# Kernel tuning notes

Measured on AMD Instinct MI355X. Metric: run time of the kernel, lower is better.

The kernel has to match this reference:

```python
import jax, jax.numpy as jnp
import numpy as np

N_NODES = 100000
N_EDGES = 3200000
NFEAT, NHID, NCLASS = 256, 128, 16


def setup_inputs() -> dict:
    key = jax.random.key(0)
    ks = jax.random.split(key, 7)
    features = jax.random.normal(ks[0], (N_NODES, NFEAT), dtype=jnp.float32)
    edge_index = jax.random.randint(ks[1], (2, N_EDGES), 0, N_NODES, dtype=jnp.int32)
    edge_weight = jax.random.uniform(ks[2], (N_EDGES,), dtype=jnp.float32)
    s1 = 1.0 / np.sqrt(NFEAT)
    s2 = 1.0 / np.sqrt(NHID)
    W1 = jax.random.uniform(ks[3], (NFEAT, NHID), dtype=jnp.float32, minval=-s1, maxval=s1)
    b1 = jax.random.uniform(ks[4], (NHID,), dtype=jnp.float32, minval=-s1, maxval=s1)
    W2 = jax.random.uniform(ks[5], (NHID, NCLASS), dtype=jnp.float32, minval=-s2, maxval=s2)
    b2 = jax.random.uniform(ks[6], (NCLASS,), dtype=jnp.float32, minval=-s2, maxval=s2)
    return {"features": features, "edge_index": edge_index, "edge_weight": edge_weight,
            "W1": W1, "b1": b1, "W2": W2, "b2": b2}


def _sgconv(x, edge_index, edge_weight, W, b, num_nodes):
    # gcn_norm with self-loops (PyG default for SGConv, K=1)
    row, col = edge_index[0], edge_index[1]
    loop = jnp.arange(num_nodes, dtype=row.dtype)
    row = jnp.concatenate([row, loop])
    col = jnp.concatenate([col, loop])
    ew = jnp.concatenate([edge_weight, jnp.ones((num_nodes,), edge_weight.dtype)])
    deg = jax.ops.segment_sum(ew, col, num_segments=num_nodes)
    dinv = jnp.where(deg > 0, jax.lax.rsqrt(deg), 0.0)
    norm = dinv[row] * ew * dinv[col]                       # [E+N]
    msg = x[row] * norm[:, None]                            # gather + scale
    out = jax.ops.segment_sum(msg, col, num_segments=num_nodes)  # scatter-add to targets
    return out @ W + b


def reference(features, edge_index, edge_weight, W1, b1, W2, b2):
    n = features.shape[0]
    h = jax.nn.relu(_sgconv(features, edge_index, edge_weight, W1, b1, n))
    # dropout is identity in eval mode (training=False)
    h = _sgconv(h, edge_index, edge_weight, W2, b2, n)
    return jax.nn.log_softmax(h, axis=1)
```

## Files before the change

### kernel.cpp

```cpp
#include <hip/hip_runtime.h>
#include <hip/hip_bf16.h>

typedef unsigned short u16;
typedef unsigned char u8;
typedef short bf16x8 __attribute__((ext_vector_type(8)));
typedef float f32x4 __attribute__((ext_vector_type(4)));
typedef float f32x2 __attribute__((ext_vector_type(2)));

__device__ __forceinline__ float blo(unsigned u) { return __uint_as_float(u << 16); }
__device__ __forceinline__ float bhi(unsigned u) { return __uint_as_float(u & 0xFFFF0000u); }
__device__ __forceinline__ u16 f2bf(float f) {
    unsigned x = __float_as_uint(f);
    x += 0x7fffu + ((x >> 16) & 1u);
    return (u16)(x >> 16);
}
__device__ __forceinline__ u8 f2fp8(float f) {
    return (u8)(__builtin_amdgcn_cvt_pk_fp8_f32(f, f, 0, false) & 0xFF);
}

#define CAP 80
#define NB_SHIFT 7
#define BNODES 128
#define CAPB 4608
#define MAXNB 800
#define PK 136
#define EPB 4096


__global__ __launch_bounds__(256) void k_prepw(const float* __restrict__ W1, u16* __restrict__ W1t) {
    int t = blockIdx.x * 256 + threadIdx.x;
    int k = t >> 5;
    int n4 = (t & 31) * 4;
    float4 v = *(const float4*)(W1 + k * 128 + n4);
    W1t[(n4 + 0) * 256 + k] = f2bf(v.x);
    W1t[(n4 + 1) * 256 + k] = f2bf(v.y);
    W1t[(n4 + 2) * 256 + k] = f2bf(v.z);
    W1t[(n4 + 3) * 256 + k] = f2bf(v.w);
}


__global__ __launch_bounds__(512) void k_bin(const int* __restrict__ row, const int* __restrict__ col,
                                             const float* __restrict__ ew, int* __restrict__ gcount,
                                             int2* __restrict__ binned, int E, int NB) {
    __shared__ int cl[MAXNB];
    int t = threadIdx.x;
    int base = blockIdx.x * EPB;
    for (int i = t; i < NB; i += 512) cl[i] = 0;
    __syncthreads();

    int e0 = base + t * 8;
    bool full = (e0 + 8 <= E);
    int cs[8];
    if (full) {
        int4 c0 = *(const int4*)(col + e0);
        int4 c1 = *(const int4*)(col + e0 + 4);
        cs[0] = c0.x; cs[1] = c0.y; cs[2] = c0.z; cs[3] = c0.w;
        cs[4] = c1.x; cs[5] = c1.y; cs[6] = c1.z; cs[7] = c1.w;
#pragma unroll
        for (int j = 0; j < 8; ++j) atomicAdd(&cl[cs[j] >> NB_SHIFT], 1);
    } else {
#pragma unroll
        for (int j = 0; j < 8; ++j) {
            int e = e0 + j;
            cs[j] = (e < E) ? col[e] : 0;
            if (e < E) atomicAdd(&cl[cs[j] >> NB_SHIFT], 1);
        }
    }
    __syncthreads();

    for (int b = t; b < NB; b += 512) {
        int c = cl[b];
        cl[b] = (c > 0) ? atomicAdd(gcount + b, c) : 0;
    }
    __syncthreads();

    if (full) {
        int4 r0 = *(const int4*)(row + e0);
        int4 r1 = *(const int4*)(row + e0 + 4);
        float4 w0 = *(const float4*)(ew + e0);
        float4 w1 = *(const float4*)(ew + e0 + 4);
        int rs[8] = {r0.x, r0.y, r0.z, r0.w, r1.x, r1.y, r1.z, r1.w};
        float wv[8] = {w0.x, w0.y, w0.z, w0.w, w1.x, w1.y, w1.z, w1.w};
#pragma unroll
        for (int j = 0; j < 8; ++j) {
            int c = cs[j];
            int b = c >> NB_SHIFT;
            int slot = atomicAdd(&cl[b], 1);
            if (slot < CAPB)
                binned[(size_t)b * CAPB + slot] =
                    make_int2(rs[j] | ((c & (BNODES - 1)) << 20), __float_as_int(wv[j]));
        }
    } else {
#pragma unroll
        for (int j = 0; j < 8; ++j) {
            int e = e0 + j;
            if (e < E) {
                int c = cs[j];
                int b = c >> NB_SHIFT;
                int slot = atomicAdd(&cl[b], 1);
                if (slot < CAPB)
                    binned[(size_t)b * CAPB + slot] =
                        make_int2(row[e] | ((c & (BNODES - 1)) << 20), __float_as_int(ew[e]));
            }
        }
    }
}


__global__ __launch_bounds__(512) void k_fill(const int* __restrict__ gcount, const int2* __restrict__ binned,
                                              int* __restrict__ cnt, float* __restrict__ dinv,
                                              int2* __restrict__ ell, int N, int NB) {
    __shared__ int   c128[BNODES];
    __shared__ float d128[BNODES];
    int t = threadIdx.x;
    int b = blockIdx.x;
    if (t < BNODES) { c128[t] = 0; d128[t] = 0.f; }
    __syncthreads();
    int M = min(gcount[b], CAPB);
    int nb0 = b << NB_SHIFT;
    const int2* src = binned + (size_t)b * CAPB;
    for (int j = t; j < M; j += 512) {
        int2 rec = src[j];
        int r  = rec.x & 0xFFFFF;
        int lc = rec.x >> 20;
        int slot = atomicAdd(&c128[lc], 1);
        if (slot < CAP) ell[(size_t)(nb0 + lc) * CAP + slot] = make_int2(r, rec.y);
        atomicAdd(&d128[lc], __int_as_float(rec.y));
    }
    __syncthreads();
    if (t < BNODES) {
        int n = nb0 + t;
        if (n < N) {
            cnt[n]  = c128[t];
            dinv[n] = rsqrtf(1.0f + d128[t]);
        }
    }
}


__global__ __launch_bounds__(256) void k_gemm1(const float* __restrict__ feat, const u16* __restrict__ W1t,
                                               const float* __restrict__ dinv, u8* __restrict__ h0f, int N) {
    __shared__ u16 As[64 * PK];
    __shared__ u16 Bs[128 * PK];
    int t = threadIdx.x;
    int nb0 = blockIdx.x * 64;
    int wv = t >> 6, lane = t & 63;
    int m16 = lane & 15, quad = lane >> 4;

    f32x4 zero4 = {0.f, 0.f, 0.f, 0.f};
    f32x4 acc[8];
#pragma unroll
    for (int i = 0; i < 8; ++i) acc[i] = zero4;

    for (int half = 0; half < 2; ++half) {
        int k0 = half * 128;
#pragma unroll
        for (int i = 0; i < 8; ++i) {
            int idx = t + 256 * i;
            int r = idx >> 5;
            int c4 = idx & 31;
            int gn = nb0 + r;
            float4 v = (gn < N) ? *(const float4*)(feat + (size_t)gn * 256 + k0 + c4 * 4)
                                : make_float4(0.f, 0.f, 0.f, 0.f);
            ushort4 o;
            o.x = f2bf(v.x); o.y = f2bf(v.y); o.z = f2bf(v.z); o.w = f2bf(v.w);
            *(ushort4*)(As + r * PK + c4 * 4) = o;
        }
#pragma unroll
        for (int i = 0; i < 8; ++i) {
            int idx = t + 256 * i;
            int r = idx >> 4;
            int c = (idx & 15) * 8;
            *(uint4*)(Bs + r * PK + c) = *(const uint4*)(W1t + r * 256 + k0 + c);
        }
        __syncthreads();
        const u16* arow = As + (wv * 16 + m16) * PK + quad * 8;
        const u16* brow = Bs + m16 * PK + quad * 8;
#pragma unroll
        for (int kc = 0; kc < 4; ++kc) {
            bf16x8 a = *(const bf16x8*)(arow + kc * 32);
#pragma unroll
            for (int tn = 0; tn < 8; ++tn) {
                bf16x8 b = *(const bf16x8*)(brow + tn * 16 * PK + kc * 32);
                acc[tn] = __builtin_amdgcn_mfma_f32_16x16x32_bf16(a, b, acc[tn], 0, 0, 0);
            }
        }
        __syncthreads();
    }
    int node0 = nb0 + wv * 16 + quad * 4;
    float dv[4];
#pragma unroll
    for (int r = 0; r < 4; ++r) dv[r] = (node0 + r < N) ? dinv[node0 + r] : 0.f;
#pragma unroll
    for (int tn = 0; tn < 8; ++tn) {
        int hid = tn * 16 + m16;
#pragma unroll
        for (int r = 0; r < 4; ++r) {
            int gn = node0 + r;
            if (gn < N) h0f[(size_t)gn * 128 + hid] = f2fp8(acc[tn][r] * dv[r]);
        }
    }
}


__global__ __launch_bounds__(256) void k_agg1(const u8* __restrict__ h0f, const float* __restrict__ dinv,
                                              const int* __restrict__ cnt, const int2* __restrict__ ell,
                                              const float* __restrict__ b1, const float* __restrict__ W2,
                                              u16* __restrict__ h2b, int N) {
    __shared__ float s_row[16][132];
    __shared__ float s_w2[2048];
    int t = threadIdx.x;
    int wv = t >> 6, lane = t & 63;
    int g = lane >> 4;
    int fl = lane & 15;
    int f = fl * 8;
    int ln = wv * 4 + g;
    int n = blockIdx.x * 16 + ln;
    bool active = n < N;

    {
        float4 wa = *(const float4*)(W2 + t * 8);
        float4 wb = *(const float4*)(W2 + t * 8 + 4);
        *(float4*)&s_w2[t * 8]     = wa;
        *(float4*)&s_w2[t * 8 + 4] = wb;
    }

    f32x2 acc2[4];
#pragma unroll
    for (int j = 0; j < 4; ++j) acc2[j] = (f32x2){0.f, 0.f};

#define ACC8P(V, W)                                                                  \
    {                                                                                \
        f32x2 wv2 = {(W), (W)};                                                      \
        acc2[0] += __builtin_amdgcn_cvt_pk_f32_fp8((V).x, false) * wv2;              \
        acc2[1] += __builtin_amdgcn_cvt_pk_f32_fp8((V).x, true)  * wv2;              \
        acc2[2] += __builtin_amdgcn_cvt_pk_f32_fp8((V).y, false) * wv2;              \
        acc2[3] += __builtin_amdgcn_cvt_pk_f32_fp8((V).y, true)  * wv2;              \
    }

    if (active) {
        float dn = dinv[n];
        {
            uint2 sv = *(const uint2*)(h0f + (size_t)n * 128 + f);
            ACC8P(sv, dn);
        }
        int m = min(cnt[n], CAP);
        const int2* ep = ell + (size_t)n * CAP;
        int k = 0;
        for (; k + 3 < m; k += 4) {
            int4 e01 = *(const int4*)(ep + k);
            int4 e23 = *(const int4*)(ep + k + 2);
            uint2 v0 = *(const uint2*)(h0f + (size_t)e01.x * 128 + f);
            uint2 v1 = *(const uint2*)(h0f + (size_t)e01.z * 128 + f);
            uint2 v2 = *(const uint2*)(h0f + (size_t)e23.x * 128 + f);
            uint2 v3 = *(const uint2*)(h0f + (size_t)e23.z * 128 + f);
            float w0 = __int_as_float(e01.y) * dn;
            float w1 = __int_as_float(e01.w) * dn;
            float w2x = __int_as_float(e23.y) * dn;
            float w3 = __int_as_float(e23.w) * dn;
            ACC8P(v0, w0);
            ACC8P(v1, w1);
            ACC8P(v2, w2x);
            ACC8P(v3, w3);
        }
        for (; k < m; ++k) {
            int2 e = ep[k];
            float w = __int_as_float(e.y) * dn;
            uint2 v = *(const uint2*)(h0f + (size_t)e.x * 128 + f);
            ACC8P(v, w);
        }
        float4 bA = *(const float4*)(b1 + f);
        float4 bB = *(const float4*)(b1 + f + 4);
        float4 oA, oB;
        oA.x = fmaxf(acc2[0][0] + bA.x, 0.f); oA.y = fmaxf(acc2[0][1] + bA.y, 0.f);
        oA.z = fmaxf(acc2[1][0] + bA.z, 0.f); oA.w = fmaxf(acc2[1][1] + bA.w, 0.f);
        oB.x = fmaxf(acc2[2][0] + bB.x, 0.f); oB.y = fmaxf(acc2[2][1] + bB.y, 0.f);
        oB.z = fmaxf(acc2[3][0] + bB.z, 0.f); oB.w = fmaxf(acc2[3][1] + bB.w, 0.f);
        *(float4*)&s_row[ln][f]     = oA;
        *(float4*)&s_row[ln][f + 4] = oB;
    }
#undef ACC8P
    __syncthreads();

    int nn = t >> 4;
    int c = t & 15;
    int gn = blockIdx.x * 16 + nn;
    float a2 = 0.f;
#pragma unroll
    for (int k = 0; k < 128; ++k) a2 += s_row[nn][k] * s_w2[k * 16 + c];
    if (gn < N) h2b[(size_t)gn * 16 + c] = f2bf(a2 * dinv[gn]);
}


__global__ __launch_bounds__(256) void k_agg2(const u16* __restrict__ g2b, const float* __restrict__ dinv,
                                              const int* __restrict__ cnt, const int2* __restrict__ ell,
                                              const float* __restrict__ b2, float* __restrict__ out, int N) {
    int t = threadIdx.x;
    int wv = t >> 6, lane = t & 63;
    int g = lane >> 3;
    int fl = lane & 7;
    int n = blockIdx.x * 32 + wv * 8 + g;
    if (n >= N) return;
    float dn = dinv[n];
    float2 acc;
    {
        unsigned sv = *(const unsigned*)(g2b + (size_t)n * 16 + fl * 2);
        acc.x = blo(sv) * dn;
        acc.y = bhi(sv) * dn;
    }
    int m = min(cnt[n], CAP);
    const int2* ep = ell + (size_t)n * CAP;
    int k = 0;
    for (; k + 3 < m; k += 4) {
        int2 e0 = ep[k], e1 = ep[k + 1], e2 = ep[k + 2], e3 = ep[k + 3];
        unsigned v0 = *(const unsigned*)(g2b + (size_t)e0.x * 16 + fl * 2);
        unsigned v1 = *(const unsigned*)(g2b + (size_t)e1.x * 16 + fl * 2);
        unsigned v2 = *(const unsigned*)(g2b + (size_t)e2.x * 16 + fl * 2);
        unsigned v3 = *(const unsigned*)(g2b + (size_t)e3.x * 16 + fl * 2);
        float w0 = __int_as_float(e0.y) * dn;
        float w1 = __int_as_float(e1.y) * dn;
        float w2 = __int_as_float(e2.y) * dn;
        float w3 = __int_as_float(e3.y) * dn;
        acc.x += blo(v0) * w0 + blo(v1) * w1 + blo(v2) * w2 + blo(v3) * w3;
        acc.y += bhi(v0) * w0 + bhi(v1) * w1 + bhi(v2) * w2 + bhi(v3) * w3;
    }
    for (; k < m; ++k) {
        int2 e = ep[k];
        float w = __int_as_float(e.y) * dn;
        unsigned v = *(const unsigned*)(g2b + (size_t)e.x * 16 + fl * 2);
        acc.x += blo(v) * w;
        acc.y += bhi(v) * w;
    }
    float v0 = acc.x + b2[fl * 2];
    float v1 = acc.y + b2[fl * 2 + 1];
    float mx = fmaxf(v0, v1);
    mx = fmaxf(mx, __shfl_xor(mx, 1));
    mx = fmaxf(mx, __shfl_xor(mx, 2));
    mx = fmaxf(mx, __shfl_xor(mx, 4));
    float ex = __expf(v0 - mx) + __expf(v1 - mx);
    ex += __shfl_xor(ex, 1);
    ex += __shfl_xor(ex, 2);
    ex += __shfl_xor(ex, 4);
    float lse = mx + __logf(ex);
    *(float2*)(out + (size_t)n * 16 + fl * 2) = make_float2(v0 - lse, v1 - lse);
}


extern "C" void kernel_launch(void* const* d_in, const int* in_sizes, int n_in,
                              void* d_out, int out_size, void* d_ws, size_t ws_size,
                              hipStream_t stream) {
    const float* feat = (const float*)d_in[0];
    const int*   eidx = (const int*)d_in[1];
    const float* ew   = (const float*)d_in[2];
    const float* W1   = (const float*)d_in[3];
    const float* b1   = (const float*)d_in[4];
    const float* W2   = (const float*)d_in[5];
    const float* b2   = (const float*)d_in[6];
    float* out = (float*)d_out;

    int N = in_sizes[0] / 256;
    int E = in_sizes[2];
    const int* row = eidx;
    const int* col = eidx + E;
    int NB = (N + BNODES - 1) >> NB_SHIFT;

    char* ws = (char*)d_ws;
    size_t off = 0;
    auto take = [&](size_t bytes) { void* p = ws + off; off += (bytes + 255) & ~(size_t)255; return p; };
    int*   cnt    = (int*)take((size_t)N * 4);
    float* dinv   = (float*)take((size_t)N * 4);
    int*   gcount = (int*)take((size_t)NB * 4);
    u16*   W1t    = (u16*)take((size_t)128 * 256 * 2);
    int2*  ell    = (int2*)take((size_t)N * CAP * 8);
    size_t ubytes = (size_t)NB * CAPB * 8;
    size_t h0fb   = (size_t)N * 128;
    void*  uni    = take(ubytes > h0fb ? ubytes : h0fb);
    u16*   h2b    = (u16*)take((size_t)N * 16 * 2);
    int2*  binned = (int2*)uni;
    u8*    h0f    = (u8*)uni;

    auto cdiv = [](long long a, long long b) { return (int)((a + b - 1) / b); };

    hipMemsetAsync(gcount, 0, (size_t)NB * 4, stream);
    k_bin   <<<cdiv(E, EPB), 512, 0, stream>>>(row, col, ew, gcount, binned, E, NB);
    k_fill  <<<NB, 512, 0, stream>>>(gcount, binned, cnt, dinv, ell, N, NB);
    k_prepw <<<32, 256, 0, stream>>>(W1, W1t);

    k_gemm1 <<<cdiv(N, 64), 256, 0, stream>>>(feat, W1t, dinv, h0f, N);
    k_agg1  <<<cdiv(N, 16), 256, 0, stream>>>(h0f, dinv, cnt, ell, b1, W2, h2b, N);
    k_agg2  <<<cdiv(N, 32), 256, 0, stream>>>(h2b, dinv, cnt, ell, b2, out, N);
}
```

Baseline: 400.5 us.

## Stage binned edge records in shared memory for coalesced scatter writes

The binning kernel now computes a block-local prefix sum over bin counts, places each edge record into a bin-sorted shared-memory buffer along with its global destination, and then writes records out in sorted order. Consecutive threads then write consecutive slots within the same bin, replacing the random per-edge global scatter. The cost is about 56 KB of LDS per block, a 10-step scan with barriers, and lower occupancy for this kernel.

```diff
diff --git a/kernel.cpp b/kernel.cpp
--- a/kernel.cpp
+++ b/kernel.cpp
@@ -22,7 +22,6 @@
 #define NB_SHIFT 7
 #define BNODES 128
 #define CAPB 4608
-#define MAXNB 800
 #define PK 136
 #define EPB 4096
 
@@ -42,67 +41,84 @@
 __global__ __launch_bounds__(512) void k_bin(const int* __restrict__ row, const int* __restrict__ col,
                                              const float* __restrict__ ew, int* __restrict__ gcount,
                                              int2* __restrict__ binned, int E, int NB) {
-    __shared__ int cl[MAXNB];
+    __shared__ int      cl[1024];
+    __shared__ int      lpre[1024];
+    __shared__ int      lfill[1024];
+    __shared__ int2     srec[EPB];
+    __shared__ unsigned ga[EPB];
     int t = threadIdx.x;
     int base = blockIdx.x * EPB;
-    for (int i = t; i < NB; i += 512) cl[i] = 0;
+
+    for (int i = t; i < 1024; i += 512) { cl[i] = 0; lfill[i] = 0; }
+    for (int i = t; i < EPB; i += 512) ga[i] = 0xFFFFFFFFu;
     __syncthreads();
 
     int e0 = base + t * 8;
     bool full = (e0 + 8 <= E);
-    int cs[8];
+    int cs[8]; int rs[8]; float wv[8];
     if (full) {
         int4 c0 = *(const int4*)(col + e0);
         int4 c1 = *(const int4*)(col + e0 + 4);
-        cs[0] = c0.x; cs[1] = c0.y; cs[2] = c0.z; cs[3] = c0.w;
-        cs[4] = c1.x; cs[5] = c1.y; cs[6] = c1.z; cs[7] = c1.w;
-#pragma unroll
-        for (int j = 0; j < 8; ++j) atomicAdd(&cl[cs[j] >> NB_SHIFT], 1);
-    } else {
-#pragma unroll
-        for (int j = 0; j < 8; ++j) {
-            int e = e0 + j;
-            cs[j] = (e < E) ? col[e] : 0;
-            if (e < E) atomicAdd(&cl[cs[j] >> NB_SHIFT], 1);
-        }
-    }
-    __syncthreads();
-
-    for (int b = t; b < NB; b += 512) {
-        int c = cl[b];
-        cl[b] = (c > 0) ? atomicAdd(gcount + b, c) : 0;
-    }
-    __syncthreads();
-
-    if (full) {
         int4 r0 = *(const int4*)(row + e0);
         int4 r1 = *(const int4*)(row + e0 + 4);
         float4 w0 = *(const float4*)(ew + e0);
         float4 w1 = *(const float4*)(ew + e0 + 4);
-        int rs[8] = {r0.x, r0.y, r0.z, r0.w, r1.x, r1.y, r1.z, r1.w};
-        float wv[8] = {w0.x, w0.y, w0.z, w0.w, w1.x, w1.y, w1.z, w1.w};
-#pragma unroll
-        for (int j = 0; j < 8; ++j) {
-            int c = cs[j];
-            int b = c >> NB_SHIFT;
-            int slot = atomicAdd(&cl[b], 1);
-            if (slot < CAPB)
-                binned[(size_t)b * CAPB + slot] =
-                    make_int2(rs[j] | ((c & (BNODES - 1)) << 20), __float_as_int(wv[j]));
-        }
+        cs[0] = c0.x; cs[1] = c0.y; cs[2] = c0.z; cs[3] = c0.w;
+        cs[4] = c1.x; cs[5] = c1.y; cs[6] = c1.z; cs[7] = c1.w;
+        rs[0] = r0.x; rs[1] = r0.y; rs[2] = r0.z; rs[3] = r0.w;
+        rs[4] = r1.x; rs[5] = r1.y; rs[6] = r1.z; rs[7] = r1.w;
+        wv[0] = w0.x; wv[1] = w0.y; wv[2] = w0.z; wv[3] = w0.w;
+        wv[4] = w1.x; wv[5] = w1.y; wv[6] = w1.z; wv[7] = w1.w;
+#pragma unroll
+        for (int j = 0; j < 8; ++j) atomicAdd(&cl[cs[j] >> NB_SHIFT], 1);
     } else {
 #pragma unroll
         for (int j = 0; j < 8; ++j) {
             int e = e0 + j;
-            if (e < E) {
-                int c = cs[j];
-                int b = c >> NB_SHIFT;
-                int slot = atomicAdd(&cl[b], 1);
-                if (slot < CAPB)
-                    binned[(size_t)b * CAPB + slot] =
-                        make_int2(row[e] | ((c & (BNODES - 1)) << 20), __float_as_int(ew[e]));
-            }
-        }
+            bool v = e < E;
+            cs[j] = v ? col[e] : -1;
+            rs[j] = v ? row[e] : 0;
+            wv[j] = v ? ew[e] : 0.f;
+            if (v) atomicAdd(&cl[cs[j] >> NB_SHIFT], 1);
+        }
+    }
+    __syncthreads();
+
+    for (int i = t; i < 1024; i += 512) lpre[i] = cl[i];
+    __syncthreads();
+
+    for (int d = 1; d < 1024; d <<= 1) {
+        int i0 = t, i1 = t + 512;
+        int v0 = lpre[i0] + ((i0 >= d) ? lpre[i0 - d] : 0);
+        int v1 = lpre[i1] + ((i1 >= d) ? lpre[i1 - d] : 0);
+        __syncthreads();
+        lpre[i0] = v0; lpre[i1] = v1;
+        __syncthreads();
+    }
+
+    for (int b = t; b < NB; b += 512) {
+        int c = cl[b];
+        cl[b]   = (c > 0) ? atomicAdd(gcount + b, c) : 0;
+        lpre[b] -= c;
+    }
+    __syncthreads();
+
+#pragma unroll
+    for (int j = 0; j < 8; ++j) {
+        if (cs[j] >= 0) {
+            int b = cs[j] >> NB_SHIFT;
+            int ls = atomicAdd(&lfill[b], 1);
+            int idx = lpre[b] + ls;
+            int gs = cl[b] + ls;
+            srec[idx] = make_int2(rs[j] | ((cs[j] & (BNODES - 1)) << 20), __float_as_int(wv[j]));
+            ga[idx] = (gs < CAPB) ? (unsigned)(b * CAPB + gs) : 0xFFFFFFFFu;
+        }
+    }
+    __syncthreads();
+
+    for (int i = t; i < EPB; i += 512) {
+        unsigned a = ga[i];
+        if (a != 0xFFFFFFFFu) binned[a] = srec[i];
     }
 }
 
@@ -381,7 +397,7 @@
 
     auto cdiv = [](long long a, long long b) { return (int)((a + b - 1) / b); };
 
-    hipMemsetAsync(gcount, 0, (size_t)NB * 4, stream);
+    (void)hipMemsetAsync(gcount, 0, (size_t)NB * 4, stream);
     k_bin   <<<cdiv(E, EPB), 512, 0, stream>>>(row, col, ew, gcount, binned, E, NB);
     k_fill  <<<NB, 512, 0, stream>>>(gcount, binned, cnt, dinv, ell, N, NB);
     k_prepw <<<32, 256, 0, stream>>>(W1, W1t);
```

Result: faster. 370.2 us (-7.6%).
